# Performance work log

Measured on AMD Instinct MI355X. Metric: run time of the kernel, lower is better.

The kernel has to match this reference:

```python
import jax, jax.numpy as jnp
import numpy as np

ED = 200      # entity/relation dim
KW = 9        # kernel width
OC = 32       # out channels
WOUT = ED - KW + 1  # 192 valid-conv output width
B = 1024
NE = 40943
NR = 18


def setup_inputs() -> dict:
    key = jax.random.key(0)
    ks = jax.random.split(key, 9)
    g = lambda k, shape: jax.random.normal(k, shape, jnp.float32) * 0.05
    return dict(
        e1_idx=jax.random.randint(ks[0], (B,), 0, NE, dtype=jnp.int32),
        r_idx=jax.random.randint(ks[1], (B,), 0, NR, dtype=jnp.int32),
        W1=g(ks[2], (ED, KW * OC)),
        b1=g(ks[3], (KW * OC,)),
        W2=g(ks[4], (WOUT * OC, ED)),
        b2=g(ks[5], (ED,)),
        bias_logits=g(ks[6], (NE,)),
        E=g(ks[7], (NE, ED)),
        R=g(ks[8], (NR, ED)),
    )


def reference(e1_idx, r_idx, W1, b1, W2, b2, bias_logits, E, R):
    e1 = E[e1_idx]          # [B, 200]
    r = R[r_idx]            # [B, 200]
    # hypernetwork: relation -> per-sample conv filters [B, KW, OC]
    k = (r @ W1 + b1).reshape(-1, KW, OC)
    # per-sample valid 1D conv of e1 with its own filters (depthwise-as-groups trick collapsed)
    idx = jnp.arange(WOUT)[:, None] + jnp.arange(KW)[None, :]  # [WOUT, KW]
    patches = e1[:, idx]                                        # [B, WOUT, KW]
    # flatten order matches TF: (out_channel major, width minor)
    feat = jnp.einsum('bwj,bjo->bow', patches, k).reshape(e1.shape[0], OC * WOUT)
    h = jax.nn.relu(feat @ W2 + b2)                             # [B, 200]
    logits = h @ E.T + bias_logits                              # [B, NE]
    return logits
```

## Files before the change

### kernel.cpp

```cpp
#include <hip/hip_runtime.h>

#define NE 40943
#define NR 18
#define ED 200
#define KWC 9
#define OC 32
#define WOUT 192
#define KOC 288
#define KH 224
#define CONV_BLOCKS ((NE * (KH / 4) + 255) / 256)

typedef unsigned short u16;
typedef unsigned int u32;
typedef __bf16 bf16x8 __attribute__((ext_vector_type(8)));
typedef float f32x4 __attribute__((ext_vector_type(4)));
typedef u16 u16x8 __attribute__((ext_vector_type(8)));
typedef u16 u16x4 __attribute__((ext_vector_type(4)));

__device__ __forceinline__ u16 f2bf(float f) {
  u32 u = __builtin_bit_cast(u32, f);
  u32 r = (u + 0x7fffu + ((u >> 16) & 1u)) >> 16;
  return (u16)r;
}

__device__ __forceinline__ void gl_lds16(const u16* g, u16* l) {
  __builtin_amdgcn_global_load_lds(
      (const __attribute__((address_space(1))) u32*)g,
      (__attribute__((address_space(3))) u32*)l, 16, 0, 0);
}

__global__ void prep_k_kernel(const float* __restrict__ R,
                              const float* __restrict__ W1,
                              const float* __restrict__ b1,
                              float* __restrict__ KrT) {
  int rel = blockIdx.x;
  int j = threadIdx.x;
  float acc = b1[j];
  const float* rrow = R + rel * ED;
  for (int d = 0; d < ED; ++d) acc += rrow[d] * W1[d * KOC + j];
  KrT[j * NR + rel] = acc;
}

__global__ __launch_bounds__(256) void build_c_conv_kernel(const float* __restrict__ KrT,
                                                           const float* __restrict__ W2,
                                                           float* __restrict__ C,
                                                           const float* __restrict__ E,
                                                           u16* __restrict__ Eb) {
  if (blockIdx.x < ED) {
    int p = blockIdx.x;
    int d = threadIdx.x;
    int jlo = p > (WOUT - 1) ? p - (WOUT - 1) : 0;
    int jhi = p < (KWC - 1) ? p : (KWC - 1);
    if (d < ED) {
      float acc[NR];
#pragma unroll
      for (int r = 0; r < NR; ++r) acc[r] = 0.f;
      for (int j = jlo; j <= jhi; ++j) {
        int w = p - j;
        const float* w2base = W2 + (size_t)w * ED + d;
        const float* kb = KrT + (j * OC) * NR;
#pragma unroll
        for (int o = 0; o < OC; ++o) {
          float w2v = w2base[(size_t)o * WOUT * ED];
#pragma unroll
          for (int r = 0; r < NR; ++r) acc[r] += kb[o * NR + r] * w2v;
        }
      }
#pragma unroll
      for (int r = 0; r < NR; ++r) C[((size_t)r * ED + p) * ED + d] = acc[r];
    }
  } else {
    int idx = (blockIdx.x - ED) * 256 + threadIdx.x;
    const int total = NE * (KH / 4);
    if (idx >= total) return;
    int row = idx / (KH / 4);
    int c4 = (idx % (KH / 4)) * 4;
    u16x4 st = {0, 0, 0, 0};
    if (c4 < ED) {
      f32x4 v = *(const f32x4*)(E + (size_t)row * ED + c4);
      st[0] = f2bf(v[0]); st[1] = f2bf(v[1]); st[2] = f2bf(v[2]); st[3] = f2bf(v[3]);
    }
    *(u16x4*)(Eb + (size_t)row * KH + c4) = st;
  }
}

__global__ __launch_bounds__(256) void h_kernel(const int* __restrict__ e1_idx,
                                                const int* __restrict__ r_idx,
                                                const float* __restrict__ E,
                                                const float* __restrict__ C,
                                                const float* __restrict__ b2,
                                                u16* __restrict__ Hb) {
  __shared__ float e1s[ED];
  int b = blockIdx.x;
  int t = threadIdx.x;
  if (t < ED) e1s[t] = E[(size_t)e1_idx[b] * ED + t];
  __syncthreads();
  int r = r_idx[b];
  const float* Cr = C + (size_t)r * ED * ED;
  if (t < KH) {
    float acc = 0.f;
    if (t < ED) {
#pragma unroll 8
      for (int p = 0; p < ED; ++p) acc += e1s[p] * Cr[(size_t)p * ED + t];
      acc += b2[t];
      acc = acc > 0.f ? acc : 0.f;
    }
    Hb[(size_t)b * KH + t] = (t < ED) ? f2bf(acc) : (u16)0;
  }
}

__global__ __launch_bounds__(256) void gemm2_kernel(
    const u16* __restrict__ Hb,
    const u16* __restrict__ Eb,
    const float* __restrict__ bias,
    float* __restrict__ out) {
  __shared__ __align__(16) u16 lA[3][128 * 32];
  __shared__ __align__(16) u16 lB[3][128 * 32];
  const int t = threadIdx.x;
  const int wave = t >> 6, lane = t & 63;

  int id = blockIdx.x;
  int xcd = id & 7;
  int q = id >> 3;
  int bx = xcd * 40 + q % 40;
  int by = q / 40;
  const int m0 = by * 128;
  const int n0 = bx * 128;
  const int wm = (wave >> 1) * 64, wn = (wave & 1) * 64;
  const int lr = lane & 15, lq = lane >> 4;
  const int csw = (lq ^ ((lr >> 1) & 3)) * 8;

  int aoff[2], boff[2], loff[2];
#pragma unroll
  for (int s = 0; s < 2; ++s) {
    int chunk = wave * 128 + s * 64 + lane;
    int r = chunk >> 2, cc = chunk & 3;
    int ccs = cc ^ ((r >> 1) & 3);
    loff[s] = chunk * 8;
    aoff[s] = (m0 + r) * KH + ccs * 8;
    int gr = n0 + r;
    if (gr > NE - 1) gr = NE - 1;
    boff[s] = gr * KH + ccs * 8;
  }

  f32x4 zero = {0.f, 0.f, 0.f, 0.f};
  f32x4 acc[4][4];
#pragma unroll
  for (int i = 0; i < 4; ++i)
#pragma unroll
    for (int j = 0; j < 4; ++j) acc[i][j] = zero;

#define GSTAGE(kt, c)                                      \
  do {                                                     \
    gl_lds16(Hb + aoff[0] + (kt) * 32, &lA[c][loff[0]]);   \
    gl_lds16(Eb + boff[0] + (kt) * 32, &lB[c][loff[0]]);   \
    gl_lds16(Hb + aoff[1] + (kt) * 32, &lA[c][loff[1]]);   \
    gl_lds16(Eb + boff[1] + (kt) * 32, &lB[c][loff[1]]);   \
  } while (0)

#define WAIT_SB(n)                                         \
  do {                                                     \
    asm volatile("s_waitcnt vmcnt(" #n ")" ::: "memory");  \
    __builtin_amdgcn_sched_barrier(0);                     \
    __builtin_amdgcn_s_barrier();                          \
    __builtin_amdgcn_sched_barrier(0);                     \
  } while (0)

#define KITER(kt, cur, dostage)                                                   \
  do {                                                                            \
    bf16x8 af[4], bfv[4];                                                         \
    _Pragma("unroll") for (int mi = 0; mi < 4; ++mi)                              \
        af[mi] = *(const bf16x8*)(&lA[cur][(wm + mi * 16 + lr) * 32 + csw]);      \
    _Pragma("unroll") for (int ni = 0; ni < 4; ++ni)                              \
        bfv[ni] = *(const bf16x8*)(&lB[cur][(wn + ni * 16 + lr) * 32 + csw]);     \
    asm volatile("s_waitcnt lgkmcnt(0)" ::: "memory");                            \
    __builtin_amdgcn_sched_barrier(0);                                            \
    __builtin_amdgcn_s_barrier();                                                 \
    __builtin_amdgcn_sched_barrier(0);                                            \
    if (dostage) GSTAGE((kt) + 3, cur);                                           \
    __builtin_amdgcn_s_setprio(1);                                                \
    _Pragma("unroll") for (int mi = 0; mi < 4; ++mi)                              \
        _Pragma("unroll") for (int ni = 0; ni < 4; ++ni)                          \
            acc[mi][ni] = __builtin_amdgcn_mfma_f32_16x16x32_bf16(                \
                af[mi], bfv[ni], acc[mi][ni], 0, 0, 0);                           \
    __builtin_amdgcn_s_setprio(0);                                                \
  } while (0)

  GSTAGE(0, 0);
  GSTAGE(1, 1);
  GSTAGE(2, 2);
  WAIT_SB(8);

  KITER(0, 0, 1); WAIT_SB(8);
  KITER(1, 1, 1); WAIT_SB(8);
  KITER(2, 2, 1); WAIT_SB(8);
  KITER(3, 0, 1); WAIT_SB(8);
  KITER(4, 1, 0); WAIT_SB(4);
  KITER(5, 2, 0); WAIT_SB(0);
  KITER(6, 0, 0);

#undef KITER
#undef WAIT_SB
#undef GSTAGE

#pragma unroll
  for (int mi = 0; mi < 4; ++mi) {
    int row = m0 + wm + mi * 16 + lq * 4;
#pragma unroll
    for (int ni = 0; ni < 4; ++ni) {
      int col = n0 + wn + ni * 16 + lr;
      if (col < NE) {
        float bv = bias[col];
#pragma unroll
        for (int i = 0; i < 4; ++i)
          out[(size_t)(row + i) * NE + col] = acc[mi][ni][i] + bv;
      }
    }
  }
}

extern "C" void kernel_launch(void* const* d_in, const int* in_sizes, int n_in,
                              void* d_out, int out_size, void* d_ws, size_t ws_size,
                              hipStream_t stream) {
  const int* e1_idx = (const int*)d_in[0];
  const int* r_idx = (const int*)d_in[1];
  const float* W1 = (const float*)d_in[2];
  const float* b1 = (const float*)d_in[3];
  const float* W2 = (const float*)d_in[4];
  const float* b2 = (const float*)d_in[5];
  const float* bias_logits = (const float*)d_in[6];
  const float* E = (const float*)d_in[7];
  const float* R = (const float*)d_in[8];
  float* out = (float*)d_out;

  char* ws = (char*)d_ws;
  float* KrT = (float*)ws;
  float* C = (float*)(ws + 32768);
  u16* Hb = (u16*)(ws + 32768 + 2880000);
  u16* Eb = (u16*)(ws + 32768 + 2880000 + 458752);

  prep_k_kernel<<<dim3(NR), dim3(KOC), 0, stream>>>(R, W1, b1, KrT);
  build_c_conv_kernel<<<dim3(ED + CONV_BLOCKS), dim3(256), 0, stream>>>(KrT, W2, C, E, Eb);
  h_kernel<<<dim3(1024), dim3(256), 0, stream>>>(e1_idx, r_idx, E, C, b2, Hb);
  gemm2_kernel<<<dim3(320 * 8), dim3(256), 0, stream>>>(Hb, Eb, bias_logits, out);
}
```

Baseline: 290.9 us.

## Fuse relation-filter prep into C-build kernel and split h-kernel accumulators

Removes the separate prep_k launch by having each of the first 200 blocks of the build kernel recompute the full relation-filter table (R·W1+b1) into shared memory. The block size rises to 288 to cover all filter columns. This removes one kernel launch and its serialization, at the cost of redundant per-block work (200×18×288×200 FMAs). The h_kernel reduction now uses four independent accumulators for more ILP, and the GEMM epilogue hoists bias loads and reorders stores row-major.

Result: slower. 328.9 us (+13.1%).

```diff
diff --git a/kernel.cpp b/kernel.cpp
--- a/kernel.cpp
+++ b/kernel.cpp
@@ -8,7 +8,7 @@
 #define WOUT 192
 #define KOC 288
 #define KH 224
-#define CONV_BLOCKS ((NE * (KH / 4) + 255) / 256)
+#define CONV_BLOCKS ((NE * (KH / 4) + 287) / 288)
 
 typedef unsigned short u16;
 typedef unsigned int u32;
@@ -29,28 +29,34 @@
       (__attribute__((address_space(3))) u32*)l, 16, 0, 0);
 }
 
-__global__ void prep_k_kernel(const float* __restrict__ R,
-                              const float* __restrict__ W1,
-                              const float* __restrict__ b1,
-                              float* __restrict__ KrT) {
-  int rel = blockIdx.x;
-  int j = threadIdx.x;
-  float acc = b1[j];
-  const float* rrow = R + rel * ED;
-  for (int d = 0; d < ED; ++d) acc += rrow[d] * W1[d * KOC + j];
-  KrT[j * NR + rel] = acc;
-}
-
-__global__ __launch_bounds__(256) void build_c_conv_kernel(const float* __restrict__ KrT,
+__global__ __launch_bounds__(288) void build_c_conv_kernel(const float* __restrict__ R,
+                                                           const float* __restrict__ W1,
+                                                           const float* __restrict__ b1,
                                                            const float* __restrict__ W2,
                                                            float* __restrict__ C,
                                                            const float* __restrict__ E,
                                                            u16* __restrict__ Eb) {
+  __shared__ float krt[KOC * NR];
   if (blockIdx.x < ED) {
-    int p = blockIdx.x;
-    int d = threadIdx.x;
-    int jlo = p > (WOUT - 1) ? p - (WOUT - 1) : 0;
-    int jhi = p < (KWC - 1) ? p : (KWC - 1);
+    const int t = threadIdx.x;
+    {
+      float acc[NR];
+#pragma unroll
+      for (int r = 0; r < NR; ++r) acc[r] = 0.f;
+      for (int d = 0; d < ED; ++d) {
+        float w1v = W1[d * KOC + t];
+#pragma unroll
+        for (int r = 0; r < NR; ++r) acc[r] += R[r * ED + d] * w1v;
+      }
+      float b1v = b1[t];
+#pragma unroll
+      for (int r = 0; r < NR; ++r) krt[t * NR + r] = acc[r] + b1v;
+    }
+    __syncthreads();
+    const int p = blockIdx.x;
+    const int d = t;
+    const int jlo = p > (WOUT - 1) ? p - (WOUT - 1) : 0;
+    const int jhi = p < (KWC - 1) ? p : (KWC - 1);
     if (d < ED) {
       float acc[NR];
 #pragma unroll
@@ -58,7 +64,7 @@
       for (int j = jlo; j <= jhi; ++j) {
         int w = p - j;
         const float* w2base = W2 + (size_t)w * ED + d;
-        const float* kb = KrT + (j * OC) * NR;
+        const float* kb = krt + (j * OC) * NR;
 #pragma unroll
         for (int o = 0; o < OC; ++o) {
           float w2v = w2base[(size_t)o * WOUT * ED];
@@ -70,7 +76,7 @@
       for (int r = 0; r < NR; ++r) C[((size_t)r * ED + p) * ED + d] = acc[r];
     }
   } else {
-    int idx = (blockIdx.x - ED) * 256 + threadIdx.x;
+    int idx = (blockIdx.x - ED) * 288 + threadIdx.x;
     const int total = NE * (KH / 4);
     if (idx >= total) return;
     int row = idx / (KH / 4);
@@ -100,9 +106,15 @@
   if (t < KH) {
     float acc = 0.f;
     if (t < ED) {
-#pragma unroll 8
-      for (int p = 0; p < ED; ++p) acc += e1s[p] * Cr[(size_t)p * ED + t];
-      acc += b2[t];
+      float a0 = 0.f, a1 = 0.f, a2 = 0.f, a3 = 0.f;
+#pragma unroll 4
+      for (int p = 0; p < ED; p += 4) {
+        a0 += e1s[p + 0] * Cr[(size_t)(p + 0) * ED + t];
+        a1 += e1s[p + 1] * Cr[(size_t)(p + 1) * ED + t];
+        a2 += e1s[p + 2] * Cr[(size_t)(p + 2) * ED + t];
+        a3 += e1s[p + 3] * Cr[(size_t)(p + 3) * ED + t];
+      }
+      acc = ((a0 + a1) + (a2 + a3)) + b2[t];
       acc = acc > 0.f ? acc : 0.f;
     }
     Hb[(size_t)b * KH + t] = (t < ED) ? f2bf(acc) : (u16)0;
@@ -203,17 +215,24 @@
 #undef WAIT_SB
 #undef GSTAGE
 
+  float bv[4];
+  bool cok[4];
+  int cols[4];
+#pragma unroll
+  for (int ni = 0; ni < 4; ++ni) {
+    cols[ni] = n0 + wn + ni * 16 + lr;
+    cok[ni] = cols[ni] < NE;
+    bv[ni] = cok[ni] ? bias[cols[ni]] : 0.f;
+  }
 #pragma unroll
   for (int mi = 0; mi < 4; ++mi) {
     int row = m0 + wm + mi * 16 + lq * 4;
 #pragma unroll
-    for (int ni = 0; ni < 4; ++ni) {
-      int col = n0 + wn + ni * 16 + lr;
-      if (col < NE) {
-        float bv = bias[col];
-#pragma unroll
-        for (int i = 0; i < 4; ++i)
-          out[(size_t)(row + i) * NE + col] = acc[mi][ni][i] + bv;
+    for (int i = 0; i < 4; ++i) {
+      size_t rb = (size_t)(row + i) * NE;
+#pragma unroll
+      for (int ni = 0; ni < 4; ++ni) {
+        if (cok[ni]) out[rb + cols[ni]] = acc[mi][ni][i] + bv[ni];
       }
     }
   }
@@ -234,13 +253,11 @@
   float* out = (float*)d_out;
 
   char* ws = (char*)d_ws;
-  float* KrT = (float*)ws;
   float* C = (float*)(ws + 32768);
   u16* Hb = (u16*)(ws + 32768 + 2880000);
   u16* Eb = (u16*)(ws + 32768 + 2880000 + 458752);
 
-  prep_k_kernel<<<dim3(NR), dim3(KOC), 0, stream>>>(R, W1, b1, KrT);
-  build_c_conv_kernel<<<dim3(ED + CONV_BLOCKS), dim3(256), 0, stream>>>(KrT, W2, C, E, Eb);
+  build_c_conv_kernel<<<dim3(ED + CONV_BLOCKS), dim3(288), 0, stream>>>(R, W1, b1, W2, C, E, Eb);
   h_kernel<<<dim3(1024), dim3(256), 0, stream>>>(e1_idx, r_idx, E, C, b2, Hb);
   gemm2_kernel<<<dim3(320 * 8), dim3(256), 0, stream>>>(Hb, Eb, bias_logits, out);
 }
```
